# Kernel tuning notes

Hardware: AMD Instinct MI355X
Metric: run time of the kernel (lower is better)

## Reference

```python
import jax, jax.numpy as jnp
import numpy as np

C = 256
HEADS = 8
HEAD_DIM = C // HEADS
GROUPS = 8
EPS = 1e-5


def setup_inputs() -> dict:
    key = jax.random.key(0)
    ks = jax.random.split(key, 11)
    B, S = 2, 16
    s = 0.02
    return {
        "x": jax.random.normal(ks[0], (B, C, S, S, S), dtype=jnp.float32),
        "gn_w": jnp.ones((C,), jnp.float32),
        "gn_b": jnp.zeros((C,), jnp.float32),
        "wq": jax.random.normal(ks[1], (C, C), jnp.float32) * s,
        "bq": jnp.zeros((C,), jnp.float32),
        "wk": jax.random.normal(ks[2], (C, C), jnp.float32) * s,
        "bk": jnp.zeros((C,), jnp.float32),
        "wv": jax.random.normal(ks[3], (C, C), jnp.float32) * s,
        "bv": jnp.zeros((C,), jnp.float32),
        "wo": jax.random.normal(ks[4], (C, C), jnp.float32) * s,
        "bo": jnp.zeros((C,), jnp.float32),
    }


def _group_norm(x, w, b):
    # x: [B, C, D, H, W]; GroupNorm(8, C) with affine params
    B, Cc, D, H, W = x.shape
    xg = x.reshape(B, GROUPS, Cc // GROUPS, D, H, W)
    mu = jnp.mean(xg, axis=(2, 3, 4, 5), keepdims=True)
    var = jnp.mean(jnp.square(xg - mu), axis=(2, 3, 4, 5), keepdims=True)
    xn = ((xg - mu) * jax.lax.rsqrt(var + EPS)).reshape(B, Cc, D, H, W)
    return xn * w[None, :, None, None, None] + b[None, :, None, None, None]


def reference(x, gn_w, gn_b, wq, bq, wk, bk, wv, bv, wo, bo):
    B, Cc, D, H, W = x.shape
    N = D * H * W
    xn = _group_norm(x, gn_w, gn_b).reshape(B, Cc, N)  # [B,C,N]
    # 1x1x1 Conv3d == per-voxel linear: weight [out,in]
    Q = jnp.einsum("oc,bcn->bon", wq, xn) + bq[None, :, None]
    K = jnp.einsum("oc,bcn->bon", wk, xn) + bk[None, :, None]
    V = jnp.einsum("oc,bcn->bon", wv, xn) + bv[None, :, None]
    Q = Q.reshape(B, HEADS, HEAD_DIM, N)
    K = K.reshape(B, HEADS, HEAD_DIM, N)
    V = V.reshape(B, HEADS, HEAD_DIM, N)
    scale = np.sqrt(HEAD_DIM).astype(np.float32)
    attn = jnp.einsum("bhdn,bhdm->bhnm", Q, K) / scale
    attn = jax.nn.softmax(attn, axis=-1)
    out = jnp.einsum("bhnm,bhdm->bhdn", attn, V)  # [B,h,hd,N]
    out = out.reshape(B, Cc, N)
    out = jnp.einsum("oc,bcn->bon", wo, out) + bo[None, :, None]
    return x + out.reshape(B, Cc, D, H, W)
```

## Files before the change

kernel.cpp:

```cpp
#include <hip/hip_runtime.h>

#define B_   2
#define C_   256
#define N_   4096
#define H_   8
#define HD_  32
#define G_   8
#define CPG_ 32

typedef short short8 __attribute__((ext_vector_type(8)));
typedef short short4v __attribute__((ext_vector_type(4)));
typedef unsigned uint4v __attribute__((ext_vector_type(4)));
typedef float f32x4  __attribute__((ext_vector_type(4)));
typedef float f4     __attribute__((ext_vector_type(4)));

__device__ __forceinline__ float b2f(short s) {
    return __uint_as_float(((unsigned)(unsigned short)s) << 16);
}
__device__ __forceinline__ short f2b(float f) {
    unsigned u = __float_as_uint(f);
    unsigned r = (u + 0x7FFF + ((u >> 16) & 1)) >> 16;
    return (short)r;
}

__global__ __launch_bounds__(256) void gn_part(const float* __restrict__ x,
                                               float* __restrict__ part) {
    int blk = blockIdx.x;
    const f4* p = (const f4*)x + (size_t)(blk >> 6) * (CPG_ * N_ / 4) + (size_t)(blk & 63) * 512;
    float s = 0.f, ss = 0.f;
#pragma unroll
    for (int i = 0; i < 2; i++) {
        f4 v = p[threadIdx.x + i * 256];
#pragma unroll
        for (int j = 0; j < 4; j++) { float f = v[j]; s += f; ss += f * f; }
    }
#pragma unroll
    for (int off = 32; off > 0; off >>= 1) {
        s  += __shfl_down(s, off);
        ss += __shfl_down(ss, off);
    }
    __shared__ float rs[4], rss[4];
    int w = threadIdx.x >> 6;
    if ((threadIdx.x & 63) == 0) { rs[w] = s; rss[w] = ss; }
    __syncthreads();
    if (threadIdx.x == 0) {
        part[blk * 2]     = rs[0] + rs[1] + rs[2] + rs[3];
        part[blk * 2 + 1] = rss[0] + rss[1] + rss[2] + rss[3];
    }
}

__global__ __launch_bounds__(256) void wconv(const float* __restrict__ wq,
                                             const float* __restrict__ wk,
                                             const float* __restrict__ wv,
                                             const float* __restrict__ wo,
                                             short* __restrict__ wb) {
    int gid = blockIdx.x * 256 + threadIdx.x;
    int rid = gid >> 13;
    int off = (gid & 8191) * 8;
    const float* src = rid == 0 ? wq : (rid == 1 ? wk : (rid == 2 ? wv : wo));
    f4 a = *(const f4*)(src + off);
    f4 b = *(const f4*)(src + off + 4);
    short8 r;
#pragma unroll
    for (int j = 0; j < 4; j++) { r[j] = f2b(a[j]); r[j + 4] = f2b(b[j]); }
    *(short8*)&wb[(size_t)rid * 65536 + off] = r;
}

__global__ __launch_bounds__(256, 2) void gemm_qkv(
    const float* __restrict__ x,
    const float* __restrict__ gw, const float* __restrict__ gb,
    const float* __restrict__ part,
    const short* __restrict__ wb,
    const float* __restrict__ bq, const float* __restrict__ bk,
    const float* __restrict__ bv,
    short* __restrict__ q, short* __restrict__ kt, short* __restrict__ v) {
    int b = blockIdx.z;
    int o0 = blockIdx.y * 64, n0 = blockIdx.x * 64;
    const float mul = 0.17677669529663687f * 1.4426950408889634f;

    __shared__ short wl[3][64][40];
    __shared__ short xl[64][40];
    __shared__ float ga[256], gbb[256];
    __shared__ float mus[8], rstds[8];

    int tid = threadIdx.x;
    int w = tid >> 6, lane = tid & 63, li = lane & 15, quad = lane >> 4;
    int wr = w & 1, wc = w >> 1;

#pragma unroll
    for (int gi = 0; gi < 2; gi++) {
        int g = w * 2 + gi;
        const float* pp = &part[(size_t)(b * 8 + g) * 128 + lane * 2];
        float s = pp[0], ss = pp[1];
#pragma unroll
        for (int off = 32; off > 0; off >>= 1) {
            s  += __shfl_down(s, off);
            ss += __shfl_down(ss, off);
        }
        if (lane == 0) {
            const float inv = 1.f / (float)(CPG_ * N_);
            float mu = s * inv;
            float var = ss * inv - mu * mu;
            mus[g] = mu;
            rstds[g] = rsqrtf(var + 1e-5f);
        }
    }
    __syncthreads();
    {
        int c = tid, g = c >> 5;
        float a = rstds[g] * gw[c];
        ga[c]  = a;
        gbb[c] = gb[c] - mus[g] * a;
    }

    f32x4 aq[2][2], ak[2][2], av[2][2];
#pragma unroll
    for (int i = 0; i < 2; i++)
#pragma unroll
        for (int j = 0; j < 2; j++) {
            aq[i][j] = (f32x4){0.f, 0.f, 0.f, 0.f};
            ak[i][j] = (f32x4){0.f, 0.f, 0.f, 0.f};
            av[i][j] = (f32x4){0.f, 0.f, 0.f, 0.f};
        }

    int wrow = tid >> 2, wco = (tid & 3) << 3;
    int cpair = tid >> 4, l16 = tid & 15;
    __syncthreads();

    for (int k0 = 0; k0 < 256; k0 += 32) {
#pragma unroll
        for (int m = 0; m < 3; m++)
            *(short8*)&wl[m][wrow][wco] =
                *(const short8*)&wb[(size_t)m * 65536 + (size_t)(o0 + wrow) * 256 + k0 + wco];
        {
            int c0 = k0 + cpair * 2;
            float a0 = ga[c0],     b0c = gbb[c0];
            float a1 = ga[c0 + 1], b1c = gbb[c0 + 1];
            const float* xr0 = x + ((size_t)(b * 256 + c0)) * N_ + n0 + l16;
            const float* xr1 = xr0 + N_;
#pragma unroll
            for (int j = 0; j < 4; j++) {
                unsigned lo = (unsigned short)f2b(xr0[16 * j] * a0 + b0c);
                unsigned hi = (unsigned short)f2b(xr1[16 * j] * a1 + b1c);
                *(unsigned*)&xl[l16 + 16 * j][cpair * 2] = lo | (hi << 16);
            }
        }
        __syncthreads();

        short8 xf[2];
#pragma unroll
        for (int i = 0; i < 2; i++)
            xf[i] = *(short8*)&xl[wc * 32 + i * 16 + li][quad * 8];
#pragma unroll
        for (int j = 0; j < 2; j++) {
            short8 wfq = *(short8*)&wl[0][wr * 32 + j * 16 + li][quad * 8];
            short8 wfk = *(short8*)&wl[1][wr * 32 + j * 16 + li][quad * 8];
            short8 wfv = *(short8*)&wl[2][wr * 32 + j * 16 + li][quad * 8];
#pragma unroll
            for (int i = 0; i < 2; i++) {
                aq[i][j] = __builtin_amdgcn_mfma_f32_16x16x32_bf16(xf[i], wfq, aq[i][j], 0, 0, 0);
                ak[i][j] = __builtin_amdgcn_mfma_f32_16x16x32_bf16(xf[i], wfk, ak[i][j], 0, 0, 0);
                av[j][i] = __builtin_amdgcn_mfma_f32_16x16x32_bf16(wfv, xf[i], av[j][i], 0, 0, 0);
            }
        }
        __syncthreads();
    }

    {
        short* outp = q + (size_t)b * N_ * C_;
#pragma unroll
        for (int i = 0; i < 2; i++) {
            int nb_ = n0 + wc * 32 + i * 16 + quad * 4;
#pragma unroll
            for (int j = 0; j < 2; j++) {
                int o_ = o0 + wr * 32 + j * 16 + li;
                float bv_ = bq[o_];
#pragma unroll
                for (int r = 0; r < 4; r++)
                    outp[(size_t)(nb_ + r) * C_ + o_] = f2b((aq[i][j][r] + bv_) * mul);
            }
        }
    }
    {
#pragma unroll
        for (int i = 0; i < 2; i++) {
            int nb_ = n0 + wc * 32 + i * 16 + quad * 4;
#pragma unroll
            for (int j = 0; j < 2; j++) {
                int o_ = o0 + wr * 32 + j * 16 + li;
                int hh = o_ >> 5, d = o_ & 31;
                float bv_ = bk[o_];
                short* kdst = kt + ((size_t)(b * 8 + hh) * N_) * HD_ + d;
#pragma unroll
                for (int r = 0; r < 4; r++)
                    kdst[(size_t)(nb_ + r) * HD_] = f2b(ak[i][j][r] + bv_);
            }
        }
    }
    {
        short* outp = v + (size_t)b * C_ * N_;
#pragma unroll
        for (int j = 0; j < 2; j++) {
            int ob = o0 + wr * 32 + j * 16 + quad * 4;
#pragma unroll
            for (int i = 0; i < 2; i++) {
                int n_ = n0 + wc * 32 + i * 16 + li;
#pragma unroll
                for (int r = 0; r < 4; r++)
                    outp[(size_t)(ob + r) * N_ + n_] = f2b(av[j][i][r] + bv[ob + r]);
            }
        }
    }
}

__global__ __launch_bounds__(512) void flash(const short* __restrict__ q,
                                             const short* __restrict__ ktp,
                                             const short* __restrict__ v,
                                             short* __restrict__ aoT) {
    int bid = blockIdx.x;
    int xcd = bid & 7;
    int rest = bid >> 3;
    int bh = xcd * 2 + (rest & 1);
    int nb = rest >> 1;
    int b = bh >> 3, h = bh & 7;

    const short* QT = q   + (size_t)b * N_ * C_ + h * HD_;
    const short* KP = ktp + (size_t)bh * N_ * HD_;
    const short* V  = v   + ((size_t)b * C_ + h * HD_) * N_;
    short* O = aoT + (size_t)b * N_ * C_ + h * HD_;

    __shared__ short kl[2 * 2560];
    __shared__ short vl[2 * 2304];

    int tid = threadIdx.x, w = tid >> 6, lane = tid & 63, li = lane & 15, quad = lane >> 4;
    int n0w = nb * 256 + w * 32;

    short8 qf0 = *(const short8*)&QT[(size_t)(n0w + li) * 256 + quad * 8];
    short8 qf1 = *(const short8*)&QT[(size_t)(n0w + 16 + li) * 256 + quad * 8];

    f32x4 oa00 = (f32x4){0.f,0.f,0.f,0.f}, oa01 = oa00, oa10 = oa00, oa11 = oa00;
    float lr0 = 0.f, lr1 = 0.f;
    const f32x4 zero = (f32x4){0.f, 0.f, 0.f, 0.f};

    int krow = tid >> 3, kcol = (tid & 7) << 2;
    const short* kgp = KP + (size_t)krow * HD_ + kcol;
    int klo = krow * 40 + kcol;
    int vd = tid >> 4, g = tid & 15;
    int mbase = 32 * (g >> 3) + 16 * (g & 1) + 4 * ((g >> 1) & 3);
    const short* vgp = V + (size_t)vd * N_ + mbase;
    int vlo = vd * 72 + g * 4;

    short4v kst = *(const short4v*)kgp;
    short4v vst = *(const short4v*)vgp;

    f32x4 s0[4], s1[4];
    short8 vf[4];

    for (int t = 0; t < 64; ++t) {
        int buf = t & 1;
        *(short4v*)&kl[buf * 2560 + klo] = kst;
        *(short4v*)&vl[buf * 2304 + vlo] = vst;
        if (t < 63) {
            kst = *(const short4v*)(kgp + (size_t)(t + 1) * 64 * HD_);
            vst = *(const short4v*)(vgp + (t + 1) * 64);
        }
        __syncthreads();

        __builtin_amdgcn_s_setprio(1);
#pragma unroll
        for (int c = 0; c < 4; c++) {
            short8 kf = *(short8*)&kl[buf * 2560 + (c * 16 + li) * 40 + quad * 8];
            s0[c] = __builtin_amdgcn_mfma_f32_16x16x32_bf16(kf, qf0, zero, 0, 0, 0);
            s1[c] = __builtin_amdgcn_mfma_f32_16x16x32_bf16(kf, qf1, zero, 0, 0, 0);
        }
        __builtin_amdgcn_s_setprio(0);

        vf[0] = *(short8*)&vl[buf * 2304 + li * 72 + quad * 8];
        vf[1] = *(short8*)&vl[buf * 2304 + (16 + li) * 72 + quad * 8];
        vf[2] = *(short8*)&vl[buf * 2304 + li * 72 + 32 + quad * 8];
        vf[3] = *(short8*)&vl[buf * 2304 + (16 + li) * 72 + 32 + quad * 8];

        unsigned paw[8];
        float lp = 0.f;
#pragma unroll
        for (int c = 0; c < 4; c++) {
            float e0 = __builtin_amdgcn_exp2f(s0[c][0]);
            float e1 = __builtin_amdgcn_exp2f(s0[c][1]);
            float e2 = __builtin_amdgcn_exp2f(s0[c][2]);
            float e3 = __builtin_amdgcn_exp2f(s0[c][3]);
            lp += (e0 + e1) + (e2 + e3);
            paw[2 * c]     = __builtin_amdgcn_perm(__float_as_uint(e1), __float_as_uint(e0), 0x07060302);
            paw[2 * c + 1] = __builtin_amdgcn_perm(__float_as_uint(e3), __float_as_uint(e2), 0x07060302);
        }
        lr0 += lp;
        uint4v p0 = (uint4v){paw[0], paw[1], paw[2], paw[3]};
        uint4v p1 = (uint4v){paw[4], paw[5], paw[6], paw[7]};
        short8 a0 = __builtin_bit_cast(short8, p0);
        short8 a1 = __builtin_bit_cast(short8, p1);

        lp = 0.f;
#pragma unroll
        for (int c = 0; c < 4; c++) {
            float e0 = __builtin_amdgcn_exp2f(s1[c][0]);
            float e1 = __builtin_amdgcn_exp2f(s1[c][1]);
            float e2 = __builtin_amdgcn_exp2f(s1[c][2]);
            float e3 = __builtin_amdgcn_exp2f(s1[c][3]);
            lp += (e0 + e1) + (e2 + e3);
            paw[2 * c]     = __builtin_amdgcn_perm(__float_as_uint(e1), __float_as_uint(e0), 0x07060302);
            paw[2 * c + 1] = __builtin_amdgcn_perm(__float_as_uint(e3), __float_as_uint(e2), 0x07060302);
        }
        lr1 += lp;
        uint4v p2 = (uint4v){paw[0], paw[1], paw[2], paw[3]};
        uint4v p3 = (uint4v){paw[4], paw[5], paw[6], paw[7]};
        short8 a2 = __builtin_bit_cast(short8, p2);
        short8 a3 = __builtin_bit_cast(short8, p3);

        __builtin_amdgcn_s_setprio(1);
        oa00 = __builtin_amdgcn_mfma_f32_16x16x32_bf16(a0, vf[0], oa00, 0, 0, 0);
        oa01 = __builtin_amdgcn_mfma_f32_16x16x32_bf16(a0, vf[1], oa01, 0, 0, 0);
        oa00 = __builtin_amdgcn_mfma_f32_16x16x32_bf16(a1, vf[2], oa00, 0, 0, 0);
        oa01 = __builtin_amdgcn_mfma_f32_16x16x32_bf16(a1, vf[3], oa01, 0, 0, 0);
        oa10 = __builtin_amdgcn_mfma_f32_16x16x32_bf16(a2, vf[0], oa10, 0, 0, 0);
        oa11 = __builtin_amdgcn_mfma_f32_16x16x32_bf16(a2, vf[1], oa11, 0, 0, 0);
        oa10 = __builtin_amdgcn_mfma_f32_16x16x32_bf16(a3, vf[2], oa10, 0, 0, 0);
        oa11 = __builtin_amdgcn_mfma_f32_16x16x32_bf16(a3, vf[3], oa11, 0, 0, 0);
        __builtin_amdgcn_s_setprio(0);
    }

    lr0 += __shfl_xor(lr0, 16); lr0 += __shfl_xor(lr0, 32);
    lr1 += __shfl_xor(lr1, 16); lr1 += __shfl_xor(lr1, 32);
#pragma unroll
    for (int r = 0; r < 4; r++) {
        float ln0 = __shfl(lr0, quad * 4 + r);
        float inv0 = 1.f / ln0;
        size_t n_ = (size_t)(n0w + quad * 4 + r);
        O[n_ * 256 + li]      = f2b(oa00[r] * inv0);
        O[n_ * 256 + 16 + li] = f2b(oa01[r] * inv0);
        float ln1 = __shfl(lr1, quad * 4 + r);
        float inv1 = 1.f / ln1;
        size_t n2 = (size_t)(n0w + 16 + quad * 4 + r);
        O[n2 * 256 + li]      = f2b(oa10[r] * inv1);
        O[n2 * 256 + 16 + li] = f2b(oa11[r] * inv1);
    }
}

__global__ __launch_bounds__(256) void gemm_out(const short* __restrict__ wob,
                                                const float* __restrict__ bias,
                                                const short* __restrict__ aoT,
                                                const float* __restrict__ resid,
                                                float* __restrict__ out) {
    int b = blockIdx.z;
    const short* X = aoT + (size_t)b * N_ * C_;
    const float* R = resid + (size_t)b * C_ * N_;
    float* outp = out + (size_t)b * C_ * N_;

    __shared__ short wl[64][40];
    __shared__ short xl[64][40];

    int o0 = blockIdx.y * 64, n0 = blockIdx.x * 64;
    int tid = threadIdx.x;
    int w = tid >> 6, lane = tid & 63, li = lane & 15, quad = lane >> 4;
    int wr = w & 1, wc = w >> 1;

    f32x4 acc[2][2];
#pragma unroll
    for (int i = 0; i < 2; i++)
#pragma unroll
        for (int j = 0; j < 2; j++) acc[i][j] = (f32x4){0.f, 0.f, 0.f, 0.f};

    int row = tid >> 2, co = (tid & 3) << 3;
    for (int k0 = 0; k0 < 256; k0 += 32) {
        *(short8*)&wl[row][co] = *(const short8*)&wob[(size_t)(o0 + row) * 256 + k0 + co];
        *(short8*)&xl[row][co] = *(const short8*)&X[(size_t)(n0 + row) * 256 + k0 + co];
        __syncthreads();
        short8 af[2], bfr[2];
#pragma unroll
        for (int i = 0; i < 2; i++) af[i]  = *(short8*)&wl[wr * 32 + i * 16 + li][quad * 8];
#pragma unroll
        for (int j = 0; j < 2; j++) bfr[j] = *(short8*)&xl[wc * 32 + j * 16 + li][quad * 8];
#pragma unroll
        for (int i = 0; i < 2; i++)
#pragma unroll
            for (int j = 0; j < 2; j++)
                acc[i][j] = __builtin_amdgcn_mfma_f32_16x16x32_bf16(af[i], bfr[j], acc[i][j], 0, 0, 0);
        __syncthreads();
    }
#pragma unroll
    for (int i = 0; i < 2; i++) {
        int ob = o0 + wr * 32 + i * 16 + quad * 4;
#pragma unroll
        for (int j = 0; j < 2; j++) {
            int n_ = n0 + wc * 32 + j * 16 + li;
#pragma unroll
            for (int r = 0; r < 4; r++) {
                size_t idx = (size_t)(ob + r) * N_ + n_;
                outp[idx] = acc[i][j][r] + bias[ob + r] + R[idx];
            }
        }
    }
}

extern "C" void kernel_launch(void* const* d_in, const int* in_sizes, int n_in,
                              void* d_out, int out_size, void* d_ws, size_t ws_size,
                              hipStream_t stream) {
    const float* x  = (const float*)d_in[0];
    const float* gw = (const float*)d_in[1];
    const float* gb = (const float*)d_in[2];
    const float* wq = (const float*)d_in[3];
    const float* bq = (const float*)d_in[4];
    const float* wk = (const float*)d_in[5];
    const float* bk = (const float*)d_in[6];
    const float* wv = (const float*)d_in[7];
    const float* bv = (const float*)d_in[8];
    const float* wo = (const float*)d_in[9];
    const float* bo = (const float*)d_in[10];
    float* out = (float*)d_out;

    char* ws = (char*)d_ws;
    float* part = (float*)ws;
    const size_t TS = (size_t)B_ * N_ * C_;
    short* aoT = (short*)(ws + 16384);
    short* q   = aoT + TS;
    short* kt  = q + TS;
    short* v   = kt + TS;
    short* wb  = v + TS;

    gn_part<<<1024, 256, 0, stream>>>(x, part);
    wconv<<<128, 256, 0, stream>>>(wq, wk, wv, wo, wb);
    gemm_qkv<<<dim3(64, 4, 2), 256, 0, stream>>>(x, gw, gb, part, wb,
                                                 bq, bk, bv, q, kt, v);
    flash<<<256, 512, 0, stream>>>(q, kt, v, aoT);
    gemm_out<<<dim3(64, 4, 2), 256, 0, stream>>>(wb + 3 * 65536, bo, aoT, x, out);
}
```

Before: 147.7 us.

## Merge GN-stats and weight-convert kernels; retile QKV GEMM to full output width

Fuses the group-norm partial-sum kernel and the weight bf16 conversion into one launch, removing one kernel launch. Retiles the QKV projection so each 512-thread block covers all 768 output channels for 32 voxels. Each x tile is then normalized and loaded once instead of four times across output-channel blocks. In exchange every block reloads the full weight slice per k-step into a larger LDS buffer, and the grid shrinks to 256 blocks, which may lower occupancy.

```diff
diff --git a/kernel.cpp b/kernel.cpp
--- a/kernel.cpp
+++ b/kernel.cpp
@@ -23,50 +23,51 @@
     return (short)r;
 }
 
-__global__ __launch_bounds__(256) void gn_part(const float* __restrict__ x,
-                                               float* __restrict__ part) {
+__global__ __launch_bounds__(256) void prep(const float* __restrict__ x,
+                                            float* __restrict__ part,
+                                            const float* __restrict__ wq,
+                                            const float* __restrict__ wk,
+                                            const float* __restrict__ wv,
+                                            const float* __restrict__ wo,
+                                            short* __restrict__ wb) {
     int blk = blockIdx.x;
-    const f4* p = (const f4*)x + (size_t)(blk >> 6) * (CPG_ * N_ / 4) + (size_t)(blk & 63) * 512;
-    float s = 0.f, ss = 0.f;
-#pragma unroll
-    for (int i = 0; i < 2; i++) {
-        f4 v = p[threadIdx.x + i * 256];
-#pragma unroll
-        for (int j = 0; j < 4; j++) { float f = v[j]; s += f; ss += f * f; }
-    }
-#pragma unroll
-    for (int off = 32; off > 0; off >>= 1) {
-        s  += __shfl_down(s, off);
-        ss += __shfl_down(ss, off);
-    }
-    __shared__ float rs[4], rss[4];
-    int w = threadIdx.x >> 6;
-    if ((threadIdx.x & 63) == 0) { rs[w] = s; rss[w] = ss; }
-    __syncthreads();
-    if (threadIdx.x == 0) {
-        part[blk * 2]     = rs[0] + rs[1] + rs[2] + rs[3];
-        part[blk * 2 + 1] = rss[0] + rss[1] + rss[2] + rss[3];
-    }
-}
-
-__global__ __launch_bounds__(256) void wconv(const float* __restrict__ wq,
-                                             const float* __restrict__ wk,
-                                             const float* __restrict__ wv,
-                                             const float* __restrict__ wo,
-                                             short* __restrict__ wb) {
-    int gid = blockIdx.x * 256 + threadIdx.x;
-    int rid = gid >> 13;
-    int off = (gid & 8191) * 8;
-    const float* src = rid == 0 ? wq : (rid == 1 ? wk : (rid == 2 ? wv : wo));
-    f4 a = *(const f4*)(src + off);
-    f4 b = *(const f4*)(src + off + 4);
-    short8 r;
-#pragma unroll
-    for (int j = 0; j < 4; j++) { r[j] = f2b(a[j]); r[j + 4] = f2b(b[j]); }
-    *(short8*)&wb[(size_t)rid * 65536 + off] = r;
-}
-
-__global__ __launch_bounds__(256, 2) void gemm_qkv(
+    if (blk < 1024) {
+        const f4* p = (const f4*)x + (size_t)(blk >> 6) * (CPG_ * N_ / 4) + (size_t)(blk & 63) * 512;
+        float s = 0.f, ss = 0.f;
+#pragma unroll
+        for (int i = 0; i < 2; i++) {
+            f4 v = p[threadIdx.x + i * 256];
+#pragma unroll
+            for (int j = 0; j < 4; j++) { float f = v[j]; s += f; ss += f * f; }
+        }
+#pragma unroll
+        for (int off = 32; off > 0; off >>= 1) {
+            s  += __shfl_down(s, off);
+            ss += __shfl_down(ss, off);
+        }
+        __shared__ float rs[4], rss[4];
+        int w = threadIdx.x >> 6;
+        if ((threadIdx.x & 63) == 0) { rs[w] = s; rss[w] = ss; }
+        __syncthreads();
+        if (threadIdx.x == 0) {
+            part[blk * 2]     = rs[0] + rs[1] + rs[2] + rs[3];
+            part[blk * 2 + 1] = rss[0] + rss[1] + rss[2] + rss[3];
+        }
+    } else {
+        int gid = (blk - 1024) * 256 + threadIdx.x;
+        int rid = gid >> 13;
+        int off = (gid & 8191) * 8;
+        const float* src = rid == 0 ? wq : (rid == 1 ? wk : (rid == 2 ? wv : wo));
+        f4 a = *(const f4*)(src + off);
+        f4 b = *(const f4*)(src + off + 4);
+        short8 r;
+#pragma unroll
+        for (int j = 0; j < 4; j++) { r[j] = f2b(a[j]); r[j + 4] = f2b(b[j]); }
+        *(short8*)&wb[(size_t)rid * 65536 + off] = r;
+    }
+}
+
+__global__ __launch_bounds__(512) void gemm_qkv(
     const float* __restrict__ x,
     const float* __restrict__ gw, const float* __restrict__ gb,
     const float* __restrict__ part,
@@ -74,23 +75,18 @@
     const float* __restrict__ bq, const float* __restrict__ bk,
     const float* __restrict__ bv,
     short* __restrict__ q, short* __restrict__ kt, short* __restrict__ v) {
-    int b = blockIdx.z;
-    int o0 = blockIdx.y * 64, n0 = blockIdx.x * 64;
+    int b = blockIdx.y;
+    int n0 = blockIdx.x * 32;
     const float mul = 0.17677669529663687f * 1.4426950408889634f;
 
-    __shared__ short wl[3][64][40];
-    __shared__ short xl[64][40];
-    __shared__ float ga[256], gbb[256];
+    __shared__ short wl[768][40];
+    __shared__ short xl[32][40];
     __shared__ float mus[8], rstds[8];
 
-    int tid = threadIdx.x;
-    int w = tid >> 6, lane = tid & 63, li = lane & 15, quad = lane >> 4;
-    int wr = w & 1, wc = w >> 1;
-
-#pragma unroll
-    for (int gi = 0; gi < 2; gi++) {
-        int g = w * 2 + gi;
-        const float* pp = &part[(size_t)(b * 8 + g) * 128 + lane * 2];
+    int tid = threadIdx.x, w = tid >> 6, lane = tid & 63, li = lane & 15, quad = lane >> 4;
+
+    {
+        const float* pp = &part[(size_t)(b * 8 + w) * 128 + lane * 2];
         float s = pp[0], ss = pp[1];
 #pragma unroll
         for (int off = 32; off > 0; off >>= 1) {
@@ -101,113 +97,94 @@
             const float inv = 1.f / (float)(CPG_ * N_);
             float mu = s * inv;
             float var = ss * inv - mu * mu;
-            mus[g] = mu;
-            rstds[g] = rsqrtf(var + 1e-5f);
+            mus[w] = mu;
+            rstds[w] = rsqrtf(var + 1e-5f);
         }
     }
     __syncthreads();
-    {
-        int c = tid, g = c >> 5;
-        float a = rstds[g] * gw[c];
-        ga[c]  = a;
-        gbb[c] = gb[c] - mus[g] * a;
-    }
-
-    f32x4 aq[2][2], ak[2][2], av[2][2];
-#pragma unroll
-    for (int i = 0; i < 2; i++)
-#pragma unroll
-        for (int j = 0; j < 2; j++) {
-            aq[i][j] = (f32x4){0.f, 0.f, 0.f, 0.f};
-            ak[i][j] = (f32x4){0.f, 0.f, 0.f, 0.f};
-            av[i][j] = (f32x4){0.f, 0.f, 0.f, 0.f};
-        }
-
-    int wrow = tid >> 2, wco = (tid & 3) << 3;
-    int cpair = tid >> 4, l16 = tid & 15;
-    __syncthreads();
+
+    f32x4 acc[6][2];
+#pragma unroll
+    for (int i = 0; i < 6; i++)
+#pragma unroll
+        for (int j = 0; j < 2; j++) acc[i][j] = (f32x4){0.f, 0.f, 0.f, 0.f};
+
+    int cpair = tid >> 5, ln = tid & 31;
+    int OW = w * 96;
 
     for (int k0 = 0; k0 < 256; k0 += 32) {
 #pragma unroll
-        for (int m = 0; m < 3; m++)
-            *(short8*)&wl[m][wrow][wco] =
-                *(const short8*)&wb[(size_t)m * 65536 + (size_t)(o0 + wrow) * 256 + k0 + wco];
+        for (int s = 0; s < 6; s++) {
+            int id = tid + 512 * s;
+            int row = id >> 2, kc = (id & 3) << 3;
+            *(short8*)&wl[row][kc] = *(const short8*)&wb[(size_t)row * 256 + k0 + kc];
+        }
         {
             int c0 = k0 + cpair * 2;
-            float a0 = ga[c0],     b0c = gbb[c0];
-            float a1 = ga[c0 + 1], b1c = gbb[c0 + 1];
-            const float* xr0 = x + ((size_t)(b * 256 + c0)) * N_ + n0 + l16;
-            const float* xr1 = xr0 + N_;
-#pragma unroll
-            for (int j = 0; j < 4; j++) {
-                unsigned lo = (unsigned short)f2b(xr0[16 * j] * a0 + b0c);
-                unsigned hi = (unsigned short)f2b(xr1[16 * j] * a1 + b1c);
-                *(unsigned*)&xl[l16 + 16 * j][cpair * 2] = lo | (hi << 16);
+            int g0 = c0 >> 5;
+            float rs_ = rstds[g0], mu_ = mus[g0];
+            float a0 = rs_ * gw[c0],     b0 = gb[c0]     - mu_ * a0;
+            float a1 = rs_ * gw[c0 + 1], b1 = gb[c0 + 1] - mu_ * a1;
+            float v0 = x[((size_t)(b * 256 + c0)) * N_ + n0 + ln] * a0 + b0;
+            float v1 = x[((size_t)(b * 256 + c0 + 1)) * N_ + n0 + ln] * a1 + b1;
+            unsigned pk = (unsigned)(unsigned short)f2b(v0) |
+                          ((unsigned)(unsigned short)f2b(v1) << 16);
+            *(unsigned*)&xl[ln][cpair * 2] = pk;
+        }
+        __syncthreads();
+
+        short8 xf0 = *(short8*)&xl[li][quad * 8];
+        short8 xf1 = *(short8*)&xl[16 + li][quad * 8];
+#pragma unroll
+        for (int i = 0; i < 6; i++) {
+            short8 wf = *(short8*)&wl[OW + i * 16 + li][quad * 8];
+            if (OW + 16 * i < 512) {
+                acc[i][0] = __builtin_amdgcn_mfma_f32_16x16x32_bf16(xf0, wf, acc[i][0], 0, 0, 0);
+                acc[i][1] = __builtin_amdgcn_mfma_f32_16x16x32_bf16(xf1, wf, acc[i][1], 0, 0, 0);
+            } else {
+                acc[i][0] = __builtin_amdgcn_mfma_f32_16x16x32_bf16(wf, xf0, acc[i][0], 0, 0, 0);
+                acc[i][1] = __builtin_amdgcn_mfma_f32_16x16x32_bf16(wf, xf1, acc[i][1], 0, 0, 0);
             }
         }
         __syncthreads();
-
-        short8 xf[2];
-#pragma unroll
-        for (int i = 0; i < 2; i++)
-            xf[i] = *(short8*)&xl[wc * 32 + i * 16 + li][quad * 8];
-#pragma unroll
-        for (int j = 0; j < 2; j++) {
-            short8 wfq = *(short8*)&wl[0][wr * 32 + j * 16 + li][quad * 8];
-            short8 wfk = *(short8*)&wl[1][wr * 32 + j * 16 + li][quad * 8];
-            short8 wfv = *(short8*)&wl[2][wr * 32 + j * 16 + li][quad * 8];
-#pragma unroll
-            for (int i = 0; i < 2; i++) {
-                aq[i][j] = __builtin_amdgcn_mfma_f32_16x16x32_bf16(xf[i], wfq, aq[i][j], 0, 0, 0);
-                ak[i][j] = __builtin_amdgcn_mfma_f32_16x16x32_bf16(xf[i], wfk, ak[i][j], 0, 0, 0);
-                av[j][i] = __builtin_amdgcn_mfma_f32_16x16x32_bf16(wfv, xf[i], av[j][i], 0, 0, 0);
+    }
+
+#pragma unroll
+    for (int i = 0; i < 6; i++) {
+        int ob = OW + i * 16;
+        int m = ob >> 8, om = ob & 255;
+        if (m == 0) {
+            short* outp = q + (size_t)b * N_ * C_;
+            int o_ = om + li;
+            float bv_ = bq[o_];
+#pragma unroll
+            for (int j = 0; j < 2; j++) {
+                int nb_ = n0 + j * 16 + quad * 4;
+#pragma unroll
+                for (int r = 0; r < 4; r++)
+                    outp[(size_t)(nb_ + r) * C_ + o_] = f2b((acc[i][j][r] + bv_) * mul);
             }
-        }
-        __syncthreads();
-    }
-
-    {
-        short* outp = q + (size_t)b * N_ * C_;
-#pragma unroll
-        for (int i = 0; i < 2; i++) {
-            int nb_ = n0 + wc * 32 + i * 16 + quad * 4;
+        } else if (m == 1) {
+            int o_ = om + li;
+            int hh = o_ >> 5, d = o_ & 31;
+            float bv_ = bk[o_];
+            short* kdst = kt + ((size_t)(b * 8 + hh) * N_) * HD_ + d;
 #pragma unroll
             for (int j = 0; j < 2; j++) {
-                int o_ = o0 + wr * 32 + j * 16 + li;
-                float bv_ = bq[o_];
+                int nb_ = n0 + j * 16 + quad * 4;
 #pragma unroll
                 for (int r = 0; r < 4; r++)
-                    outp[(size_t)(nb_ + r) * C_ + o_] = f2b((aq[i][j][r] + bv_) * mul);
+                    kdst[(size_t)(nb_ + r) * HD_] = f2b(acc[i][j][r] + bv_);
             }
-        }
-    }
-    {
-#pragma unroll
-        for (int i = 0; i < 2; i++) {
-            int nb_ = n0 + wc * 32 + i * 16 + quad * 4;
+        } else {
+            short* outp = v + (size_t)b * C_ * N_;
+            int obv = om + quad * 4;
 #pragma unroll
             for (int j = 0; j < 2; j++) {
-                int o_ = o0 + wr * 32 + j * 16 + li;
-                int hh = o_ >> 5, d = o_ & 31;
-                float bv_ = bk[o_];
-                short* kdst = kt + ((size_t)(b * 8 + hh) * N_) * HD_ + d;
+                int n_ = n0 + j * 16 + li;
 #pragma unroll
                 for (int r = 0; r < 4; r++)
-                    kdst[(size_t)(nb_ + r) * HD_] = f2b(ak[i][j][r] + bv_);
-            }
-        }
-    }
-    {
-        short* outp = v + (size_t)b * C_ * N_;
-#pragma unroll
-        for (int j = 0; j < 2; j++) {
-            int ob = o0 + wr * 32 + j * 16 + quad * 4;
-#pragma unroll
-            for (int i = 0; i < 2; i++) {
-                int n_ = n0 + wc * 32 + i * 16 + li;
-#pragma unroll
-                for (int r = 0; r < 4; r++)
-                    outp[(size_t)(ob + r) * N_ + n_] = f2b(av[j][i][r] + bv[ob + r]);
+                    outp[(size_t)(obv + r) * N_ + n_] = f2b(acc[i][j][r] + bv[obv + r]);
             }
         }
     }
@@ -425,10 +402,9 @@
     short* v   = kt + TS;
     short* wb  = v + TS;
 
-    gn_part<<<1024, 256, 0, stream>>>(x, part);
-    wconv<<<128, 256, 0, stream>>>(wq, wk, wv, wo, wb);
-    gemm_qkv<<<dim3(64, 4, 2), 256, 0, stream>>>(x, gw, gb, part, wb,
-                                                 bq, bk, bv, q, kt, v);
+    prep<<<1152, 256, 0, stream>>>(x, part, wq, wk, wv, wo, wb);
+    gemm_qkv<<<dim3(128, 2), 512, 0, stream>>>(x, gw, gb, part, wb,
+                                               bq, bk, bv, q, kt, v);
     flash<<<256, 512, 0, stream>>>(q, kt, v, aoT);
     gemm_out<<<dim3(64, 4, 2), 256, 0, stream>>>(wb + 3 * 65536, bo, aoT, x, out);
 }
```

New measurement: 152.5 us. 3.2% more time.
